# Kernel optimization log

Hardware: AMD Instinct MI355X
Metric: run time of the kernel (lower is better)

The kernel has to match this reference:

```python
import jax, jax.numpy as jnp
import numpy as np

FP8_MAX = 448.0  # float8_e4m3fn max representable value


def _fp8_quant(v):
    """Snap values to the fp8 e4m3 grid (saturating), return fp32."""
    v = jnp.clip(v, -FP8_MAX, FP8_MAX)
    return v.astype(jnp.float8_e4m3fn).astype(jnp.float32)


def setup_inputs() -> dict:
    key = jax.random.key(0)
    k1, k2, k3 = jax.random.split(key, 3)
    N_TOK, D_IN, D_OUT = 8192, 4096, 4096
    x = jax.random.normal(k1, (N_TOK, D_IN), dtype=jnp.float32)
    # weight is stored already quantized to fp8 in the real module; snap to grid
    w = jax.random.normal(k2, (D_OUT, D_IN), dtype=jnp.float32)
    weight_scale = jnp.array([2.0 / FP8_MAX], dtype=jnp.float32)  # per-tensor
    weight = _fp8_quant(w / weight_scale)  # fp8-grid values, kept in fp32
    bias = jax.random.normal(k3, (D_OUT,), dtype=jnp.float32)
    input_scale = jnp.array([4.0 / FP8_MAX], dtype=jnp.float32)  # per-tensor act scale
    return {"x": x, "weight": weight, "weight_scale": weight_scale,
            "bias": bias, "input_scale": input_scale}


def reference(x, weight, weight_scale, bias, input_scale):
    # quantize_activation_per_tensor_fp8: x/scale -> clamp -> fp8 e4m3
    qinput = _fp8_quant(x / input_scale)  # [N, D_in], fp8-grid values
    acc = jnp.einsum('nk,ok->no', qinput, weight)  # fp32 accumulate
    out = acc * (input_scale * weight_scale) + bias
    return out.astype(x.dtype)
```

## Files before the change

### kernel.cpp

```cpp
#include <hip/hip_runtime.h>
#include <stdint.h>

#define FP8_MAX 448.0f

typedef float floatx16 __attribute__((ext_vector_type(16)));
typedef int   intx4    __attribute__((ext_vector_type(4)));
typedef int   intx8    __attribute__((ext_vector_type(8)));

__device__ __forceinline__ void async_copy16(const void* g, void* s) {
    __builtin_amdgcn_global_load_lds(
        (const __attribute__((address_space(1))) void*)g,
        (__attribute__((address_space(3))) void*)s,
        16, 0, 0);
}

__global__ void __launch_bounds__(256) quant_fp8_kernel(
    const float* __restrict__ x, const float* __restrict__ w,
    const float* __restrict__ scale,
    uint8_t* __restrict__ qx, uint8_t* __restrict__ qw,
    long nx4, long ntot4)
{
    const float invx = 1.0f / scale[0];
    const long stride = (long)gridDim.x * 256;
    for (long g = (long)blockIdx.x * 256 + threadIdx.x; g < ntot4; g += stride) {
        const float4* src; int* dst; float inv; long idx;
        if (g < nx4) { src = (const float4*)x; dst = (int*)qx; inv = invx; idx = g; }
        else         { src = (const float4*)w; dst = (int*)qw; inv = 1.0f; idx = g - nx4; }
        float4 v = src[idx];
        float a = fminf(fmaxf(v.x * inv, -FP8_MAX), FP8_MAX);
        float b = fminf(fmaxf(v.y * inv, -FP8_MAX), FP8_MAX);
        float c = fminf(fmaxf(v.z * inv, -FP8_MAX), FP8_MAX);
        float d = fminf(fmaxf(v.w * inv, -FP8_MAX), FP8_MAX);
        int pk = 0;
        pk = __builtin_amdgcn_cvt_pk_fp8_f32(a, b, pk, false);
        pk = __builtin_amdgcn_cvt_pk_fp8_f32(c, d, pk, true);
        dst[idx] = pk;
    }
}

__global__ void __launch_bounds__(256, 2) gemm_fp8_kernel(
    const uint8_t* __restrict__ A, const uint8_t* __restrict__ B,
    const float* __restrict__ bias,
    const float* __restrict__ in_scale, const float* __restrict__ w_scale,
    float* __restrict__ C, int M, int N, int K)
{
    __shared__ __align__(16) uint8_t As[128 * 64];
    __shared__ __align__(16) uint8_t Bs[128 * 64];

    const int tid  = threadIdx.x;
    const int lane = tid & 63;
    const int wid  = tid >> 6;
    const int wm   = wid >> 1;
    const int wn   = wid & 1;
    const int m0   = blockIdx.y * 128;
    const int n0   = blockIdx.x * 128;

    const int rl = lane & 31;
    const int h  = lane >> 5;

    const int S0 = tid, S1 = tid + 256;
    const int rA0 = S0 >> 2, cA0 = ((S0 & 3) ^ (rA0 & 3)) * 16;
    const int rA1 = S1 >> 2, cA1 = ((S1 & 3) ^ (rA1 & 3)) * 16;

    const uint8_t* Ab = A + (size_t)m0 * K;
    const uint8_t* Bb = B + (size_t)n0 * K;

    floatx16 acc[2][2];
#pragma unroll
    for (int i = 0; i < 2; ++i)
#pragma unroll
        for (int j = 0; j < 2; ++j)
#pragma unroll
            for (int r = 0; r < 16; ++r) acc[i][j][r] = 0.f;

    const int ca   = ((h * 2)     ^ (rl & 3)) * 16;
    const int cb   = ((h * 2 + 1) ^ (rl & 3)) * 16;
    const int aoff = (wm * 64 + rl) * 64;
    const int boff = (wn * 64 + rl) * 64;

    const int sOne = 0x7F7F7F7F;

    for (int kt = 0; kt < K; kt += 64) {
        async_copy16(Ab + (size_t)rA0 * K + kt + cA0, As + S0 * 16);
        async_copy16(Ab + (size_t)rA1 * K + kt + cA1, As + S1 * 16);
        async_copy16(Bb + (size_t)rA0 * K + kt + cA0, Bs + S0 * 16);
        async_copy16(Bb + (size_t)rA1 * K + kt + cA1, Bs + S1 * 16);
        __syncthreads();

        intx8 av[2], bv[2];
#pragma unroll
        for (int mi = 0; mi < 2; ++mi) {
            intx4 lo = *(const intx4*)(As + aoff + mi * 2048 + ca);
            intx4 hi = *(const intx4*)(As + aoff + mi * 2048 + cb);
            av[mi] = (intx8){lo[0], lo[1], lo[2], lo[3],
                             hi[0], hi[1], hi[2], hi[3]};
        }
#pragma unroll
        for (int ni = 0; ni < 2; ++ni) {
            intx4 lo = *(const intx4*)(Bs + boff + ni * 2048 + ca);
            intx4 hi = *(const intx4*)(Bs + boff + ni * 2048 + cb);
            bv[ni] = (intx8){lo[0], lo[1], lo[2], lo[3],
                             hi[0], hi[1], hi[2], hi[3]};
        }

#pragma unroll
        for (int mi = 0; mi < 2; ++mi)
#pragma unroll
            for (int ni = 0; ni < 2; ++ni)
                acc[mi][ni] = __builtin_amdgcn_mfma_scale_f32_32x32x64_f8f6f4(
                    av[mi], bv[ni], acc[mi][ni],
                    0 , 0 ,
                    0, sOne, 0, sOne);

        __syncthreads();
    }

    const float osc = in_scale[0] * w_scale[0];

#pragma unroll
    for (int mi = 0; mi < 2; ++mi) {
#pragma unroll
        for (int ni = 0; ni < 2; ++ni) {
            const int gn = n0 + wn * 64 + ni * 32 + rl;
            const float bvv = bias[gn];
#pragma unroll
            for (int r = 0; r < 16; ++r) {
                const int row = (r & 3) + 8 * (r >> 2) + 4 * h;
                const int gm = m0 + wm * 64 + mi * 32 + row;
                C[(size_t)gm * N + gn] = acc[mi][ni][r] * osc + bvv;
            }
        }
    }
}

extern "C" void kernel_launch(void* const* d_in, const int* in_sizes, int n_in,
                              void* d_out, int out_size, void* d_ws, size_t ws_size,
                              hipStream_t stream) {
    const float* x        = (const float*)d_in[0];
    const float* weight   = (const float*)d_in[1];
    const float* w_scale  = (const float*)d_in[2];
    const float* bias     = (const float*)d_in[3];
    const float* in_scale = (const float*)d_in[4];
    float* out = (float*)d_out;

    const int N = in_sizes[3];
    const int K = in_sizes[1] / N;
    const int M = in_sizes[0] / K;

    uint8_t* qx = (uint8_t*)d_ws;
    uint8_t* qw = (uint8_t*)d_ws + (size_t)M * K;

    const long nx4   = (long)M * K / 4;
    const long ntot4 = nx4 + (long)N * K / 4;
    long blks = (ntot4 + 255) / 256; if (blks > 2048) blks = 2048;
    quant_fp8_kernel<<<(int)blks, 256, 0, stream>>>(x, weight, in_scale,
                                                    qx, qw, nx4, ntot4);

    dim3 grid(N / 128, M / 128);
    gemm_fp8_kernel<<<grid, 256, 0, stream>>>(qx, qw, bias, in_scale, w_scale,
                                              out, M, N, K);
}
```

Baseline: 420.3 us.

## Double-buffer LDS tiles and change swizzle to reduce bank conflicts

Splits the shared-memory A/B tiles into two buffers so the async global-to-LDS load of the next K slice is issued before the current slice's MFMAs. The goal is to overlap global memory latency with compute instead of stalling at a barrier every iteration. It also changes the XOR swizzle to key on (row>>1)&3 instead of row&3, so fragment reads spread across LDS banks differently. LDS use doubles to 32KB per block, which may limit occupancy. Correctness depends on the per-iteration barrier also covering completion of the prefetched copies.

Result: no change. 414.8 us (-1.3%).

```diff
diff --git a/kernel.cpp b/kernel.cpp
--- a/kernel.cpp
+++ b/kernel.cpp
@@ -44,8 +44,8 @@
     const float* __restrict__ in_scale, const float* __restrict__ w_scale,
     float* __restrict__ C, int M, int N, int K)
 {
-    __shared__ __align__(16) uint8_t As[128 * 64];
-    __shared__ __align__(16) uint8_t Bs[128 * 64];
+    __shared__ __align__(16) uint8_t As[2 * 128 * 64];
+    __shared__ __align__(16) uint8_t Bs[2 * 128 * 64];
 
     const int tid  = threadIdx.x;
     const int lane = tid & 63;
@@ -59,8 +59,8 @@
     const int h  = lane >> 5;
 
     const int S0 = tid, S1 = tid + 256;
-    const int rA0 = S0 >> 2, cA0 = ((S0 & 3) ^ (rA0 & 3)) * 16;
-    const int rA1 = S1 >> 2, cA1 = ((S1 & 3) ^ (rA1 & 3)) * 16;
+    const int rA0 = S0 >> 2, cA0 = ((S0 & 3) ^ ((S0 >> 3) & 3)) * 16;
+    const int rA1 = S1 >> 2, cA1 = ((S1 & 3) ^ ((S1 >> 3) & 3)) * 16;
 
     const uint8_t* Ab = A + (size_t)m0 * K;
     const uint8_t* Bb = B + (size_t)n0 * K;
@@ -73,32 +73,46 @@
 #pragma unroll
             for (int r = 0; r < 16; ++r) acc[i][j][r] = 0.f;
 
-    const int ca   = ((h * 2)     ^ (rl & 3)) * 16;
-    const int cb   = ((h * 2 + 1) ^ (rl & 3)) * 16;
+    const int fsw  = (rl >> 1) & 3;
+    const int ca   = ((h * 2)     ^ fsw) * 16;
+    const int cb   = ((h * 2 + 1) ^ fsw) * 16;
     const int aoff = (wm * 64 + rl) * 64;
     const int boff = (wn * 64 + rl) * 64;
 
     const int sOne = 0x7F7F7F7F;
+    const int NS = K >> 6;
 
-    for (int kt = 0; kt < K; kt += 64) {
-        async_copy16(Ab + (size_t)rA0 * K + kt + cA0, As + S0 * 16);
-        async_copy16(Ab + (size_t)rA1 * K + kt + cA1, As + S1 * 16);
-        async_copy16(Bb + (size_t)rA0 * K + kt + cA0, Bs + S0 * 16);
-        async_copy16(Bb + (size_t)rA1 * K + kt + cA1, Bs + S1 * 16);
-        __syncthreads();
+    async_copy16(Ab + (size_t)rA0 * K + cA0, As + S0 * 16);
+    async_copy16(Ab + (size_t)rA1 * K + cA1, As + S1 * 16);
+    async_copy16(Bb + (size_t)rA0 * K + cA0, Bs + S0 * 16);
+    async_copy16(Bb + (size_t)rA1 * K + cA1, Bs + S1 * 16);
+    __syncthreads();
 
+    int cur = 0;
+    for (int t = 0; t < NS; ++t) {
+        if (t + 1 < NS) {
+            const int kt = (t + 1) << 6;
+            const int nb = (cur ^ 1) * 8192;
+            async_copy16(Ab + (size_t)rA0 * K + kt + cA0, As + nb + S0 * 16);
+            async_copy16(Ab + (size_t)rA1 * K + kt + cA1, As + nb + S1 * 16);
+            async_copy16(Bb + (size_t)rA0 * K + kt + cA0, Bs + nb + S0 * 16);
+            async_copy16(Bb + (size_t)rA1 * K + kt + cA1, Bs + nb + S1 * 16);
+        }
+
+        const uint8_t* as = As + cur * 8192;
+        const uint8_t* bs = Bs + cur * 8192;
         intx8 av[2], bv[2];
 #pragma unroll
         for (int mi = 0; mi < 2; ++mi) {
-            intx4 lo = *(const intx4*)(As + aoff + mi * 2048 + ca);
-            intx4 hi = *(const intx4*)(As + aoff + mi * 2048 + cb);
+            intx4 lo = *(const intx4*)(as + aoff + mi * 2048 + ca);
+            intx4 hi = *(const intx4*)(as + aoff + mi * 2048 + cb);
             av[mi] = (intx8){lo[0], lo[1], lo[2], lo[3],
                              hi[0], hi[1], hi[2], hi[3]};
         }
 #pragma unroll
         for (int ni = 0; ni < 2; ++ni) {
-            intx4 lo = *(const intx4*)(Bs + boff + ni * 2048 + ca);
-            intx4 hi = *(const intx4*)(Bs + boff + ni * 2048 + cb);
+            intx4 lo = *(const intx4*)(bs + boff + ni * 2048 + ca);
+            intx4 hi = *(const intx4*)(bs + boff + ni * 2048 + cb);
             bv[ni] = (intx8){lo[0], lo[1], lo[2], lo[3],
                              hi[0], hi[1], hi[2], hi[3]};
         }
@@ -113,6 +127,7 @@
                     0, sOne, 0, sOne);
 
         __syncthreads();
+        cur ^= 1;
     }
 
     const float osc = in_scale[0] * w_scale[0];
```

## Pre-swizzle FP8 operands into MFMA fragment layout and load directly to registers

Applied to the files above, without the earlier changes.

The quantization kernel now writes the FP8 activations and weights in a per-32-row, per-64-K fragment layout that matches the MFMA operand layout, so each lane's 32 bytes sit contiguously. The GEMM drops LDS staging and barriers entirely and loads fragments straight from global memory into registers, double-buffered across K steps. The tile grows to 128x256 with 4x2 MFMAs per wave, and s_setprio is raised around the MFMA bursts. Each wave now re-reads the shared A tile from global memory or cache with no LDS reuse, and register pressure rises since launch bounds no longer request two blocks per CU.

Result: faster. 411.1 us (-2.2%).

```diff
diff --git a/kernel.cpp b/kernel.cpp
--- a/kernel.cpp
+++ b/kernel.cpp
@@ -7,25 +7,19 @@
 typedef int   intx4    __attribute__((ext_vector_type(4)));
 typedef int   intx8    __attribute__((ext_vector_type(8)));
 
-__device__ __forceinline__ void async_copy16(const void* g, void* s) {
-    __builtin_amdgcn_global_load_lds(
-        (const __attribute__((address_space(1))) void*)g,
-        (__attribute__((address_space(3))) void*)s,
-        16, 0, 0);
-}
-
-__global__ void __launch_bounds__(256) quant_fp8_kernel(
+__global__ void __launch_bounds__(256) quant_fp8_frag_kernel(
     const float* __restrict__ x, const float* __restrict__ w,
     const float* __restrict__ scale,
-    uint8_t* __restrict__ qx, uint8_t* __restrict__ qw,
-    long nx4, long ntot4)
+    int* __restrict__ qx, int* __restrict__ qw,
+    long nx4, long ntot4, int K, int kshift)
 {
     const float invx = 1.0f / scale[0];
+    const int rowFrags = K >> 6;
     const long stride = (long)gridDim.x * 256;
     for (long g = (long)blockIdx.x * 256 + threadIdx.x; g < ntot4; g += stride) {
         const float4* src; int* dst; float inv; long idx;
-        if (g < nx4) { src = (const float4*)x; dst = (int*)qx; inv = invx; idx = g; }
-        else         { src = (const float4*)w; dst = (int*)qw; inv = 1.0f; idx = g - nx4; }
+        if (g < nx4) { src = (const float4*)x; dst = qx; inv = invx; idx = g; }
+        else         { src = (const float4*)w; dst = qw; inv = 1.0f; idx = g - nx4; }
         float4 v = src[idx];
         float a = fminf(fmaxf(v.x * inv, -FP8_MAX), FP8_MAX);
         float b = fminf(fmaxf(v.y * inv, -FP8_MAX), FP8_MAX);
@@ -34,99 +28,108 @@
         int pk = 0;
         pk = __builtin_amdgcn_cvt_pk_fp8_f32(a, b, pk, false);
         pk = __builtin_amdgcn_cvt_pk_fp8_f32(c, d, pk, true);
-        dst[idx] = pk;
+        const long e = idx * 4;
+        const int  m = (int)(e >> kshift);
+        const int  k = (int)(e & (K - 1));
+        const int  frag = (m >> 5) * rowFrags + (k >> 6);
+        const int  lane = (m & 31) | (((k >> 5) & 1) << 5);
+        dst[frag * 512 + lane * 8 + ((k & 31) >> 2)] = pk;
     }
 }
 
-__global__ void __launch_bounds__(256, 2) gemm_fp8_kernel(
+__global__ void __launch_bounds__(256) gemm_fp8_kernel(
     const uint8_t* __restrict__ A, const uint8_t* __restrict__ B,
     const float* __restrict__ bias,
     const float* __restrict__ in_scale, const float* __restrict__ w_scale,
     float* __restrict__ C, int M, int N, int K)
 {
-    __shared__ __align__(16) uint8_t As[128 * 64];
-    __shared__ __align__(16) uint8_t Bs[128 * 64];
-
     const int tid  = threadIdx.x;
     const int lane = tid & 63;
     const int wid  = tid >> 6;
-    const int wm   = wid >> 1;
-    const int wn   = wid & 1;
     const int m0   = blockIdx.y * 128;
-    const int n0   = blockIdx.x * 128;
+    const int n0   = blockIdx.x * 256;
 
     const int rl = lane & 31;
     const int h  = lane >> 5;
 
-    const int S0 = tid, S1 = tid + 256;
-    const int rA0 = S0 >> 2, cA0 = ((S0 & 3) ^ (rA0 & 3)) * 16;
-    const int rA1 = S1 >> 2, cA1 = ((S1 & 3) ^ (rA1 & 3)) * 16;
+    const int rowFrags = K >> 6;
+    const int NS = rowFrags;
 
-    const uint8_t* Ab = A + (size_t)m0 * K;
-    const uint8_t* Bb = B + (size_t)n0 * K;
+    const uint8_t* pA[4];
+    const uint8_t* pB[2];
+#pragma unroll
+    for (int mi = 0; mi < 4; ++mi)
+        pA[mi] = A + ((size_t)((m0 >> 5) + mi) * rowFrags) * 2048 + lane * 32;
+#pragma unroll
+    for (int ni = 0; ni < 2; ++ni)
+        pB[ni] = B + ((size_t)((n0 >> 5) + wid * 2 + ni) * rowFrags) * 2048 + lane * 32;
 
-    floatx16 acc[2][2];
+    floatx16 acc[4][2];
 #pragma unroll
-    for (int i = 0; i < 2; ++i)
+    for (int i = 0; i < 4; ++i)
 #pragma unroll
         for (int j = 0; j < 2; ++j)
 #pragma unroll
             for (int r = 0; r < 16; ++r) acc[i][j][r] = 0.f;
 
-    const int ca   = ((h * 2)     ^ (rl & 3)) * 16;
-    const int cb   = ((h * 2 + 1) ^ (rl & 3)) * 16;
-    const int aoff = (wm * 64 + rl) * 64;
-    const int boff = (wn * 64 + rl) * 64;
-
     const int sOne = 0x7F7F7F7F;
 
-    for (int kt = 0; kt < K; kt += 64) {
-        async_copy16(Ab + (size_t)rA0 * K + kt + cA0, As + S0 * 16);
-        async_copy16(Ab + (size_t)rA1 * K + kt + cA1, As + S1 * 16);
-        async_copy16(Bb + (size_t)rA0 * K + kt + cA0, Bs + S0 * 16);
-        async_copy16(Bb + (size_t)rA1 * K + kt + cA1, Bs + S1 * 16);
-        __syncthreads();
-
-        intx8 av[2], bv[2];
+    auto loadA = [&](intx8* dst, int t) {
 #pragma unroll
-        for (int mi = 0; mi < 2; ++mi) {
-            intx4 lo = *(const intx4*)(As + aoff + mi * 2048 + ca);
-            intx4 hi = *(const intx4*)(As + aoff + mi * 2048 + cb);
-            av[mi] = (intx8){lo[0], lo[1], lo[2], lo[3],
-                             hi[0], hi[1], hi[2], hi[3]};
+        for (int mi = 0; mi < 4; ++mi) {
+            intx4 lo = *(const intx4*)(pA[mi] + (size_t)t * 2048);
+            intx4 hi = *(const intx4*)(pA[mi] + (size_t)t * 2048 + 16);
+            dst[mi] = (intx8){lo[0], lo[1], lo[2], lo[3],
+                              hi[0], hi[1], hi[2], hi[3]};
         }
+    };
+    auto loadB = [&](intx8* dst, int t) {
 #pragma unroll
         for (int ni = 0; ni < 2; ++ni) {
-            intx4 lo = *(const intx4*)(Bs + boff + ni * 2048 + ca);
-            intx4 hi = *(const intx4*)(Bs + boff + ni * 2048 + cb);
-            bv[ni] = (intx8){lo[0], lo[1], lo[2], lo[3],
-                             hi[0], hi[1], hi[2], hi[3]};
+            intx4 lo = *(const intx4*)(pB[ni] + (size_t)t * 2048);
+            intx4 hi = *(const intx4*)(pB[ni] + (size_t)t * 2048 + 16);
+            dst[ni] = (intx8){lo[0], lo[1], lo[2], lo[3],
+                              hi[0], hi[1], hi[2], hi[3]};
         }
+    };
+    auto mfma8 = [&](intx8* av, intx8* bv) {
+        __builtin_amdgcn_s_setprio(1);
+#pragma unroll
+        for (int mi = 0; mi < 4; ++mi) {
+            acc[mi][0] = __builtin_amdgcn_mfma_scale_f32_32x32x64_f8f6f4(
+                av[mi], bv[0], acc[mi][0], 0, 0, 0, sOne, 0, sOne);
+            acc[mi][1] = __builtin_amdgcn_mfma_scale_f32_32x32x64_f8f6f4(
+                av[mi], bv[1], acc[mi][1], 0, 0, 0, sOne, 0, sOne);
+        }
+        __builtin_amdgcn_s_setprio(0);
+    };
 
-#pragma unroll
-        for (int mi = 0; mi < 2; ++mi)
-#pragma unroll
-            for (int ni = 0; ni < 2; ++ni)
-                acc[mi][ni] = __builtin_amdgcn_mfma_scale_f32_32x32x64_f8f6f4(
-                    av[mi], bv[ni], acc[mi][ni],
-                    0 , 0 ,
-                    0, sOne, 0, sOne);
+    intx8 a0[4], b0[2], a1[4], b1[2];
+    loadA(a0, 0); loadB(b0, 0);
+    loadA(a1, 1); loadB(b1, 1);
 
-        __syncthreads();
+    int t = 0;
+    for (; t + 2 < NS; t += 2) {
+        mfma8(a0, b0);
+        loadA(a0, t + 2); loadB(b0, t + 2);
+        mfma8(a1, b1);
+        loadA(a1, t + 3); loadB(b1, t + 3);
     }
+    mfma8(a0, b0);
+    mfma8(a1, b1);
 
     const float osc = in_scale[0] * w_scale[0];
 
 #pragma unroll
-    for (int mi = 0; mi < 2; ++mi) {
+    for (int mi = 0; mi < 4; ++mi) {
 #pragma unroll
         for (int ni = 0; ni < 2; ++ni) {
-            const int gn = n0 + wn * 64 + ni * 32 + rl;
+            const int gn = n0 + wid * 64 + ni * 32 + rl;
             const float bvv = bias[gn];
 #pragma unroll
             for (int r = 0; r < 16; ++r) {
                 const int row = (r & 3) + 8 * (r >> 2) + 4 * h;
-                const int gm = m0 + wm * 64 + mi * 32 + row;
+                const int gm = m0 + mi * 32 + row;
                 C[(size_t)gm * N + gn] = acc[mi][ni][r] * osc + bvv;
             }
         }
@@ -147,16 +150,18 @@
     const int K = in_sizes[1] / N;
     const int M = in_sizes[0] / K;
 
+    int kshift = 0; while ((1 << kshift) < K) ++kshift;
+
     uint8_t* qx = (uint8_t*)d_ws;
     uint8_t* qw = (uint8_t*)d_ws + (size_t)M * K;
 
     const long nx4   = (long)M * K / 4;
     const long ntot4 = nx4 + (long)N * K / 4;
     long blks = (ntot4 + 255) / 256; if (blks > 2048) blks = 2048;
-    quant_fp8_kernel<<<(int)blks, 256, 0, stream>>>(x, weight, in_scale,
-                                                    qx, qw, nx4, ntot4);
+    quant_fp8_frag_kernel<<<(int)blks, 256, 0, stream>>>(
+        x, weight, in_scale, (int*)qx, (int*)qw, nx4, ntot4, K, kshift);
 
-    dim3 grid(N / 128, M / 128);
+    dim3 grid(N / 256, M / 128);
     gemm_fp8_kernel<<<grid, 256, 0, stream>>>(qx, qw, bias, in_scale, w_scale,
                                               out, M, N, K);
 }
```
